# Performance work log

Measured on AMD Instinct MI355X. Metric: run time of the kernel, lower is better.

The kernel has to match this reference:

```python
import jax, jax.numpy as jnp
import numpy as np

B, S, D_MODEL, D_K = 4, 2048, 1024, 1
D_QKV = D_MODEL * D_K  # per-stream feature dim (q, k, v each)
MASK_NEG = -9000000000000000.0


def setup_inputs() -> dict:
    key = jax.random.key(0)
    kx, kw = jax.random.split(key)
    x = jax.random.normal(kx, (B, S, D_MODEL), dtype=jnp.float32)
    # Dense kernel, flax convention: [in_features, out_features], no bias
    W = jax.random.normal(kw, (D_MODEL, 3 * D_QKV), dtype=jnp.float32) * (1.0 / np.sqrt(D_MODEL))
    return {"x": x, "W": W}


def _scaled_dot_product_attention(q, k, v):
    # q,k,v: [B, S, d]
    d_k = k.shape[-1]
    scores = jnp.einsum("bqd,bkd->bqk", q, k) / jnp.sqrt(jnp.float32(d_k))
    # Faithful to source: keep upper triangle (incl. diagonal), then mask zeros.
    scores = jnp.triu(scores, k=0)
    scores = jnp.where(scores == 0, MASK_NEG, scores)
    attn = jax.nn.softmax(scores, axis=-1)
    return jnp.einsum("bqk,bkd->bqd", attn, v)


def reference(x, W) -> jnp.ndarray:
    qkv = jnp.einsum("bsd,df->bsf", x, W)  # fused QKV projection
    q, k, v = jnp.split(qkv, 3, axis=-1)
    return _scaled_dot_product_attention(q, k, v)
```

## Files before the change

kernel.cpp:

```cpp
#include <hip/hip_runtime.h>

#define SB 2048
#define DM 1024
#define N3 3072

typedef short bf16x8 __attribute__((ext_vector_type(8)));
typedef float f32x4 __attribute__((ext_vector_type(4)));
typedef unsigned short u16;

#define MFMA16(a, b, c) __builtin_amdgcn_mfma_f32_16x16x32_bf16(a, b, c, 0, 0, 0)

typedef const __attribute__((address_space(1))) unsigned int* gptr_t;
typedef __attribute__((address_space(3))) unsigned int* lptr_t;

__device__ __forceinline__ u16 f2bf(float x) {
  union { float f; unsigned u; } c; c.f = x;
  unsigned r = c.u + 0x7FFFu + ((c.u >> 16) & 1u);
  return (u16)(r >> 16);
}
__device__ __forceinline__ float bf2f(u16 x) {
  union { unsigned u; float f; } c; c.u = ((unsigned)x) << 16;
  return c.f;
}
__device__ __forceinline__ void glds(const u16* g, u16* l) {
  __builtin_amdgcn_global_load_lds((gptr_t)(const void*)g, (lptr_t)(void*)l, 16, 0, 0);
}


__global__ void k_cvt_x(const float* __restrict__ x, u16* __restrict__ xb, int n4) {
  int i = blockIdx.x * blockDim.x + threadIdx.x;
  if (i >= n4) return;
  float4 v = ((const float4*)x)[i];
  ushort4 o;
  o.x = f2bf(v.x); o.y = f2bf(v.y); o.z = f2bf(v.z); o.w = f2bf(v.w);
  ((ushort4*)xb)[i] = o;
}

__global__ void k_cvt_wt(const float* __restrict__ W, u16* __restrict__ Wt) {
  __shared__ float t[32][33];
  int n0 = blockIdx.x * 32;
  int k0 = blockIdx.y * 32;
  int tx = threadIdx.x & 31, ty = threadIdx.x >> 5;
#pragma unroll
  for (int r = 0; r < 4; ++r)
    t[ty + r * 8][tx] = W[(size_t)(k0 + ty + r * 8) * N3 + n0 + tx];
  __syncthreads();
#pragma unroll
  for (int r = 0; r < 4; ++r)
    Wt[(size_t)(n0 + ty + r * 8) * DM + k0 + tx] = f2bf(t[tx][ty + r * 8]);
}

__global__ __launch_bounds__(256, 2) void k_gemm(const u16* __restrict__ xb,
                                                 const u16* __restrict__ wt,
                                                 u16* __restrict__ qk,
                                                 u16* __restrict__ vt) {
  __shared__ u16 As[2][128 * 32];
  __shared__ u16 Bs[2][128 * 32];
  int bid = blockIdx.x;
  int mt = bid / 24, nt = bid % 24;
  int m0 = mt * 128, n0 = nt * 128;
  int tid = threadIdx.x, lane = tid & 63, wid = tid >> 6;
  int lr = lane & 15, lg = lane >> 4;
  int wm = (wid >> 1) * 64, wn = (wid & 1) * 64;
  int ca = lane >> 2;
  int seg = lane & 3;

#define STAGE(pb, kk) do {                                                \
    _Pragma("unroll")                                                     \
    for (int j = 0; j < 2; ++j) {                                         \
      int chunk = wid * 2 + j;                                            \
      int row = chunk * 16 + ca;                                          \
      int scol = ((seg - (row >> 1)) & 3) * 8;                            \
      glds(xb + (size_t)(m0 + row) * 1024 + (kk) + scol, &As[pb][chunk * 512]); \
      glds(wt + (size_t)(n0 + row) * 1024 + (kk) + scol, &Bs[pb][chunk * 512]); \
    } } while (0)

  f32x4 acc[4][4] = {};
  int p = 0;
  STAGE(0, 0);
  __syncthreads();
  for (int t = 0; t < 32; ++t) {
    if (t < 31) STAGE(p ^ 1, t * 32 + 32);
    bf16x8 af[4], bff[4];
#pragma unroll
    for (int i = 0; i < 4; ++i) {
      int row = wm + i * 16 + lr;
      af[i] = *(const bf16x8*)&As[p][row * 32 + ((lg + (row >> 1)) & 3) * 8];
    }
#pragma unroll
    for (int j = 0; j < 4; ++j) {
      int row = wn + j * 16 + lr;
      bff[j] = *(const bf16x8*)&Bs[p][row * 32 + ((lg + (row >> 1)) & 3) * 8];
    }
#pragma unroll
    for (int i = 0; i < 4; ++i)
#pragma unroll
      for (int j = 0; j < 4; ++j)
        acc[i][j] = MFMA16(af[i], bff[j], acc[i][j]);
    __syncthreads();
    p ^= 1;
  }
#undef STAGE

  if (n0 < 2048) {
#pragma unroll
    for (int i = 0; i < 4; ++i)
#pragma unroll
      for (int j = 0; j < 4; ++j)
#pragma unroll
        for (int r = 0; r < 4; ++r)
          qk[(size_t)(m0 + wm + i * 16 + lg * 4 + r) * 2048 + n0 + wn + j * 16 + lr] = f2bf(acc[i][j][r]);
  } else {
#pragma unroll
    for (int i = 0; i < 4; ++i)
#pragma unroll
      for (int j = 0; j < 4; ++j)
#pragma unroll
        for (int r = 0; r < 4; ++r) {
          int m = m0 + wm + i * 16 + lg * 4 + r;
          int d = n0 + wn + j * 16 + lr - 2048;
          vt[(size_t)((m >> 11) * DM + d) * SB + (m & 2047)] = f2bf(acc[i][j][r]);
        }
  }
}

__global__ __launch_bounds__(256, 2) void k_qkt(const u16* __restrict__ qk,
                                                u16* __restrict__ S) {
  __shared__ u16 As[2][128 * 32];
  __shared__ u16 Bs[2][128 * 32];
  int bid = blockIdx.x;
  int b = bid & 3;
  int pi = bid >> 2;
  int qt = 0;
  while (true) { int cnt = 16 - qt; if (pi < cnt) break; pi -= cnt; ++qt; }
  int kt = qt + pi;
  int m0 = qt * 128, n0 = kt * 128;
  int tid = threadIdx.x, lane = tid & 63, wid = tid >> 6;
  int lr = lane & 15, lg = lane >> 4;
  int wm = (wid >> 1) * 64, wn = (wid & 1) * 64;
  int ca = lane >> 2;
  int seg = lane & 3;
  const u16* Qb = qk + (size_t)(b * SB) * 2048;

#define STAGE(pb, kk) do {                                                \
    _Pragma("unroll")                                                     \
    for (int j = 0; j < 2; ++j) {                                         \
      int chunk = wid * 2 + j;                                            \
      int row = chunk * 16 + ca;                                          \
      int scol = ((seg - (row >> 1)) & 3) * 8;                            \
      glds(Qb + (size_t)(m0 + row) * 2048 + (kk) + scol, &As[pb][chunk * 512]);        \
      glds(Qb + (size_t)(n0 + row) * 2048 + 1024 + (kk) + scol, &Bs[pb][chunk * 512]); \
    } } while (0)

  f32x4 acc[4][4] = {};
  int p = 0;
  STAGE(0, 0);
  __syncthreads();
  for (int t = 0; t < 32; ++t) {
    if (t < 31) STAGE(p ^ 1, t * 32 + 32);
    bf16x8 af[4], bff[4];
#pragma unroll
    for (int i = 0; i < 4; ++i) {
      int row = wm + i * 16 + lr;
      af[i] = *(const bf16x8*)&As[p][row * 32 + ((lg + (row >> 1)) & 3) * 8];
    }
#pragma unroll
    for (int j = 0; j < 4; ++j) {
      int row = wn + j * 16 + lr;
      bff[j] = *(const bf16x8*)&Bs[p][row * 32 + ((lg + (row >> 1)) & 3) * 8];
    }
#pragma unroll
    for (int i = 0; i < 4; ++i)
#pragma unroll
      for (int j = 0; j < 4; ++j)
        acc[i][j] = MFMA16(af[i], bff[j], acc[i][j]);
    __syncthreads();
    p ^= 1;
  }
#undef STAGE

  u16* Sb = S + (size_t)(b * SB) * 2048;
#pragma unroll
  for (int i = 0; i < 4; ++i)
#pragma unroll
    for (int j = 0; j < 4; ++j)
#pragma unroll
      for (int r = 0; r < 4; ++r) {
        int q = m0 + wm + i * 16 + lg * 4 + r;
        int k = n0 + wn + j * 16 + lr;
        float v = acc[i][j][r] * 0.03125f;
        if (k < q) v = -1e30f;
        Sb[(size_t)q * 2048 + k] = f2bf(v);
      }
}

__global__ void k_sm(u16* __restrict__ S) {
  __shared__ float rmax[4], rsum[4];
  int row = blockIdx.x;
  int q = row & 2047;
  int k0 = (q >> 7) << 7;
  int len = 2048 - k0;
  int tid = threadIdx.x;
  u16* rp = S + (size_t)row * 2048 + k0;
  int nv = len >> 3;
  bool act = tid < nv;
  float v[8];
  float mx = -1e30f;
  if (act) {
    bf16x8 x = *(const bf16x8*)(rp + tid * 8);
#pragma unroll
    for (int j = 0; j < 8; ++j) { v[j] = bf2f((u16)x[j]); mx = fmaxf(mx, v[j]); }
  }
#pragma unroll
  for (int off = 32; off; off >>= 1) mx = fmaxf(mx, __shfl_xor(mx, off, 64));
  int wv = tid >> 6;
  if ((tid & 63) == 0) rmax[wv] = mx;
  __syncthreads();
  mx = fmaxf(fmaxf(rmax[0], rmax[1]), fmaxf(rmax[2], rmax[3]));
  float sum = 0.f;
  if (act) {
#pragma unroll
    for (int j = 0; j < 8; ++j) { v[j] = __expf(v[j] - mx); sum += v[j]; }
  }
#pragma unroll
  for (int off = 32; off; off >>= 1) sum += __shfl_xor(sum, off, 64);
  if ((tid & 63) == 0) rsum[wv] = sum;
  __syncthreads();
  float inv = 1.f / ((rsum[0] + rsum[1]) + (rsum[2] + rsum[3]));
  if (act) {
    bf16x8 o;
#pragma unroll
    for (int j = 0; j < 8; ++j) o[j] = (short)f2bf(v[j] * inv);
    *(bf16x8*)(rp + tid * 8) = o;
  }
}

__global__ __launch_bounds__(256, 2) void k_pv(const u16* __restrict__ P,
                                               const u16* __restrict__ vt,
                                               float* __restrict__ out) {
  __shared__ u16 As[2][128 * 32];
  __shared__ u16 Bs[2][128 * 32];
  int bid = blockIdx.x;
  int qt = bid >> 5;
  int rem = bid & 31;
  int dt = rem >> 2;
  int b = rem & 3;
  int m0 = qt * 128, n0 = dt * 128;
  int nkt = (2048 - m0) >> 5;
  int tid = threadIdx.x, lane = tid & 63, wid = tid >> 6;
  int lr = lane & 15, lg = lane >> 4;
  int wm = (wid >> 1) * 64, wn = (wid & 1) * 64;
  int ca = lane >> 2;
  int seg = lane & 3;
  const u16* Pb = P + (size_t)(b * SB) * 2048;
  const u16* Vb = vt + (size_t)(b * DM) * 2048;

#define STAGE(pb, kk) do {                                                \
    _Pragma("unroll")                                                     \
    for (int j = 0; j < 2; ++j) {                                         \
      int chunk = wid * 2 + j;                                            \
      int row = chunk * 16 + ca;                                          \
      int scol = ((seg - (row >> 1)) & 3) * 8;                            \
      glds(Pb + (size_t)(m0 + row) * 2048 + (kk) + scol, &As[pb][chunk * 512]); \
      glds(Vb + (size_t)(n0 + row) * 2048 + (kk) + scol, &Bs[pb][chunk * 512]); \
    } } while (0)

  f32x4 acc[4][4] = {};
  int p = 0;
  STAGE(0, m0);
  __syncthreads();
  for (int t = 0; t < nkt; ++t) {
    if (t + 1 < nkt) STAGE(p ^ 1, m0 + t * 32 + 32);
    bf16x8 af[4], bff[4];
#pragma unroll
    for (int i = 0; i < 4; ++i) {
      int row = wm + i * 16 + lr;
      af[i] = *(const bf16x8*)&As[p][row * 32 + ((lg + (row >> 1)) & 3) * 8];
    }
#pragma unroll
    for (int j = 0; j < 4; ++j) {
      int row = wn + j * 16 + lr;
      bff[j] = *(const bf16x8*)&Bs[p][row * 32 + ((lg + (row >> 1)) & 3) * 8];
    }
#pragma unroll
    for (int i = 0; i < 4; ++i)
#pragma unroll
      for (int j = 0; j < 4; ++j)
        acc[i][j] = MFMA16(af[i], bff[j], acc[i][j]);
    __syncthreads();
    p ^= 1;
  }
#undef STAGE

#pragma unroll
  for (int i = 0; i < 4; ++i)
#pragma unroll
    for (int j = 0; j < 4; ++j)
#pragma unroll
      for (int r = 0; r < 4; ++r)
        out[(size_t)(b * SB + m0 + wm + i * 16 + lg * 4 + r) * DM + n0 + wn + j * 16 + lr] = acc[i][j][r];
}

extern "C" void kernel_launch(void* const* d_in, const int* in_sizes, int n_in,
                              void* d_out, int out_size, void* d_ws, size_t ws_size,
                              hipStream_t stream) {
  const float* x = (const float*)d_in[0];
  const float* W = (const float*)d_in[1];
  float* out = (float*)d_out;
  char* ws = (char*)d_ws;
  u16* qk = (u16*)(ws);
  u16* vt = (u16*)(ws + 33554432);
  u16* xb = (u16*)(ws + 50331648);
  u16* wt = (u16*)(ws + 67108864);
  u16* S  = (u16*)(ws + 50331648);

  k_cvt_x<<<8192, 256, 0, stream>>>(x, xb, 2097152);
  dim3 gw(96, 32);
  k_cvt_wt<<<gw, 256, 0, stream>>>(W, wt);
  k_gemm<<<1536, 256, 0, stream>>>(xb, wt, qk, vt);
  k_qkt<<<544, 256, 0, stream>>>(qk, S);
  k_sm<<<8192, 256, 0, stream>>>(S);
  k_pv<<<512, 256, 0, stream>>>(S, vt, out);
}
```

Measured before the change: 167.8 us.

## Merge conversion kernels and remap block indices for L2/MALL locality

```diff
diff --git a/kernel.cpp b/kernel.cpp
--- a/kernel.cpp
+++ b/kernel.cpp
@@ -27,27 +27,29 @@
 }
 
 
-__global__ void k_cvt_x(const float* __restrict__ x, u16* __restrict__ xb, int n4) {
-  int i = blockIdx.x * blockDim.x + threadIdx.x;
-  if (i >= n4) return;
-  float4 v = ((const float4*)x)[i];
-  ushort4 o;
-  o.x = f2bf(v.x); o.y = f2bf(v.y); o.z = f2bf(v.z); o.w = f2bf(v.w);
-  ((ushort4*)xb)[i] = o;
-}
-
-__global__ void k_cvt_wt(const float* __restrict__ W, u16* __restrict__ Wt) {
-  __shared__ float t[32][33];
-  int n0 = blockIdx.x * 32;
-  int k0 = blockIdx.y * 32;
-  int tx = threadIdx.x & 31, ty = threadIdx.x >> 5;
-#pragma unroll
-  for (int r = 0; r < 4; ++r)
-    t[ty + r * 8][tx] = W[(size_t)(k0 + ty + r * 8) * N3 + n0 + tx];
-  __syncthreads();
-#pragma unroll
-  for (int r = 0; r < 4; ++r)
-    Wt[(size_t)(n0 + ty + r * 8) * DM + k0 + tx] = f2bf(t[tx][ty + r * 8]);
+__global__ void k_cvt(const float* __restrict__ x, const float* __restrict__ W,
+                      u16* __restrict__ xb, u16* __restrict__ Wt) {
+  int bid = blockIdx.x;
+  if (bid < 8192) {
+    int i = bid * 256 + threadIdx.x;
+    float4 v = ((const float4*)x)[i];
+    ushort4 o;
+    o.x = f2bf(v.x); o.y = f2bf(v.y); o.z = f2bf(v.z); o.w = f2bf(v.w);
+    ((ushort4*)xb)[i] = o;
+  } else {
+    __shared__ float t[32][33];
+    int wb = bid - 8192;
+    int n0 = (wb % 96) * 32;
+    int k0 = (wb / 96) * 32;
+    int tx = threadIdx.x & 31, ty = threadIdx.x >> 5;
+#pragma unroll
+    for (int r = 0; r < 4; ++r)
+      t[ty + r * 8][tx] = W[(size_t)(k0 + ty + r * 8) * N3 + n0 + tx];
+    __syncthreads();
+#pragma unroll
+    for (int r = 0; r < 4; ++r)
+      Wt[(size_t)(n0 + ty + r * 8) * DM + k0 + tx] = f2bf(t[tx][ty + r * 8]);
+  }
 }
 
 __global__ __launch_bounds__(256, 2) void k_gemm(const u16* __restrict__ xb,
@@ -57,7 +59,8 @@
   __shared__ u16 As[2][128 * 32];
   __shared__ u16 Bs[2][128 * 32];
   int bid = blockIdx.x;
-  int mt = bid / 24, nt = bid % 24;
+  int mt = (bid & 7) * 8 + ((bid >> 3) & 7);
+  int nt = bid >> 6;
   int m0 = mt * 128, n0 = nt * 128;
   int tid = threadIdx.x, lane = tid & 63, wid = tid >> 6;
   int lr = lane & 15, lg = lane >> 4;
@@ -129,8 +132,8 @@
   __shared__ u16 As[2][128 * 32];
   __shared__ u16 Bs[2][128 * 32];
   int bid = blockIdx.x;
-  int b = bid & 3;
-  int pi = bid >> 2;
+  int b = bid / 136;
+  int pi = bid % 136;
   int qt = 0;
   while (true) { int cnt = 16 - qt; if (pi < cnt) break; pi -= cnt; ++qt; }
   int kt = qt + pi;
@@ -243,8 +246,8 @@
   int bid = blockIdx.x;
   int qt = bid >> 5;
   int rem = bid & 31;
-  int dt = rem >> 2;
-  int b = rem & 3;
+  int b = rem >> 3;
+  int dt = rem & 7;
   int m0 = qt * 128, n0 = dt * 128;
   int nkt = (2048 - m0) >> 5;
   int tid = threadIdx.x, lane = tid & 63, wid = tid >> 6;
@@ -314,9 +317,7 @@
   u16* wt = (u16*)(ws + 67108864);
   u16* S  = (u16*)(ws + 50331648);
 
-  k_cvt_x<<<8192, 256, 0, stream>>>(x, xb, 2097152);
-  dim3 gw(96, 32);
-  k_cvt_wt<<<gw, 256, 0, stream>>>(W, wt);
+  k_cvt<<<11264, 256, 0, stream>>>(x, W, xb, wt);
   k_gemm<<<1536, 256, 0, stream>>>(xb, wt, qk, vt);
   k_qkt<<<544, 256, 0, stream>>>(qk, S);
   k_sm<<<8192, 256, 0, stream>>>(S);
```

New measurement: 175.0 us. 1.04x slower.
